# Kernel optimization log

Measured on AMD Instinct MI355X. Metric: run time of the kernel, lower is better.

## Reference

```python
import jax, jax.numpy as jnp
import numpy as np

D = 256      # cfg.d_model
H = 8        # num heads
HID = D // H # head_outdim for hidden layers (32)
N = 16000    # nodes
E = 64000    # edges
NUM_GNN = 3  # cfg.num_gnn -> 2 hidden EGATConv layers + 1 final
SLOPE = 0.01 # F.leaky_relu default in DGL EGATConv


def setup_inputs() -> dict:
    key = jax.random.key(0)
    ks = jax.random.split(key, 8)
    inp = {
        "nfeat": jax.random.normal(ks[0], (N, D), jnp.float32),
        "efeat": jax.random.normal(ks[1], (E, D), jnp.float32),
        "src": jax.random.randint(ks[2], (E,), 0, N),
        "dst": jax.random.randint(ks[3], (E,), 0, N),
    }
    L = NUM_GNN - 1  # hidden layers, out_node = out_edge = HID per head
    kh = jax.random.split(ks[4], 5)
    s = 0.02
    inp["Wnode_h"] = jax.random.normal(kh[0], (L, D, H * HID), jnp.float32) * s
    inp["Wni_h"]   = jax.random.normal(kh[1], (L, D, H * HID), jnp.float32) * s
    inp["Wnj_h"]   = jax.random.normal(kh[2], (L, D, H * HID), jnp.float32) * s
    inp["Wfij_h"]  = jax.random.normal(kh[3], (L, D, H * HID), jnp.float32) * s
    inp["attn_h"]  = jax.random.normal(kh[4], (L, H, HID), jnp.float32) * s
    inp["bias_h"]  = jnp.zeros((L, H * HID), jnp.float32)
    kl = jax.random.split(ks[5], 5)
    inp["Wnode_l"] = jax.random.normal(kl[0], (D, H * D), jnp.float32) * s
    inp["Wni_l"]   = jax.random.normal(kl[1], (D, H * D), jnp.float32) * s
    inp["Wnj_l"]   = jax.random.normal(kl[2], (D, H * D), jnp.float32) * s
    inp["Wfij_l"]  = jax.random.normal(kl[3], (D, H * D), jnp.float32) * s
    inp["attn_l"]  = jax.random.normal(kl[4], (H, D), jnp.float32) * s
    inp["bias_l"]  = jnp.zeros((H * D,), jnp.float32)
    return inp


def _egat(n, f, src, dst, Wnode, Wni, Wnj, Wfij, attn, bias):
    """DGL EGATConv: edge-gated multi-head graph attention.
    n:[N,D] f:[E,D] attn:[H,od] -> (h_out:[N,H,od], f_out:[E,H,od])."""
    Hh, od = attn.shape
    # edge feature update: f_ni(u) + f_nj(v) + f_fij(e) + bias, leaky_relu
    f_out = (n @ Wni)[src] + (n @ Wnj)[dst] + f @ Wfij + bias  # [E, H*od]
    f_out = jax.nn.leaky_relu(f_out, SLOPE).reshape(-1, Hh, od)
    # attention logits + edge softmax grouped by destination node
    e = jnp.einsum('ehd,hd->eh', f_out, attn)                   # [E, H]
    m = jax.lax.stop_gradient(jax.ops.segment_max(e, dst, num_segments=N))
    ex = jnp.exp(e - m[dst])
    s = jax.ops.segment_sum(ex, dst, num_segments=N)
    a = ex / s[dst]                                             # [E, H]
    # message passing: u_mul_e + sum at dst
    h = (n @ Wnode).reshape(N, Hh, od)
    h_out = jax.ops.segment_sum(h[src] * a[..., None], dst, num_segments=N)
    return h_out, f_out


def reference(nfeat, efeat, src, dst,
              Wnode_h, Wni_h, Wnj_h, Wfij_h, attn_h, bias_h,
              Wnode_l, Wni_l, Wnj_l, Wfij_l, attn_l, bias_l):
    n, f = nfeat, efeat
    for l in range(Wnode_h.shape[0]):  # hidden layers: concat heads + ELU + residual
        tn, tf = _egat(n, f, src, dst, Wnode_h[l], Wni_h[l], Wnj_h[l],
                       Wfij_h[l], attn_h[l], bias_h[l])
        n = n + jax.nn.elu(tn.reshape(N, -1))  # reshape == concat over heads
        f = f + jax.nn.elu(tf.reshape(E, -1))
    # last layer: mean over heads + residual
    tn, tf = _egat(n, f, src, dst, Wnode_l, Wni_l, Wnj_l, Wfij_l, attn_l, bias_l)
    n = n + tn.mean(axis=1)
    f = f + tf.mean(axis=1)
    return n, f
```

## Files before the change

kernel.cpp:

```cpp
#include <hip/hip_runtime.h>

typedef unsigned short u16;
typedef __attribute__((ext_vector_type(4))) unsigned short u16x4;
typedef __attribute__((ext_vector_type(8))) unsigned short u16x8;
typedef __attribute__((ext_vector_type(4))) float f32x4;
typedef __attribute__((ext_vector_type(8))) __bf16 bf16x8;

#define NN 16000
#define NE 64000
#define ECH 16000

__device__ __forceinline__ float bf2f(u16 b) {
  union { unsigned int u; float f; } v; v.u = ((unsigned int)b) << 16; return v.f;
}
__device__ __forceinline__ u16 f2bf(float x) {
  union { float f; unsigned int u; } v; v.f = x;
  unsigned int r = v.u + 0x7FFFu + ((v.u >> 16) & 1u);
  return (u16)(r >> 16);
}

__global__ void cast_init(const float* __restrict__ in, float* __restrict__ outf,
                          u16* __restrict__ outb, int n4) {
  for (int i = blockIdx.x * blockDim.x + threadIdx.x; i < n4; i += gridDim.x * blockDim.x) {
    f32x4 v = ((const f32x4*)in)[i];
    u16x4 b;
#pragma unroll
    for (int j = 0; j < 4; ++j) b[j] = f2bf(v[j]);
    ((f32x4*)outf)[i] = v;
    ((u16x4*)outb)[i] = b;
  }
}

__global__ void cast_bf(const float* __restrict__ in, u16* __restrict__ outb, int n4) {
  for (int i = blockIdx.x * blockDim.x + threadIdx.x; i < n4; i += gridDim.x * blockDim.x) {
    f32x4 v = ((const f32x4*)in)[i];
    u16x4 b;
#pragma unroll
    for (int j = 0; j < 4; ++j) b[j] = f2bf(v[j]);
    ((u16x4*)outb)[i] = b;
  }
}

__global__ void deg_hist(const int* __restrict__ dst, int* __restrict__ deg) {
  int e = blockIdx.x * 256 + threadIdx.x;
  if (e < NE) atomicAdd(&deg[dst[e]], 1);
}

__global__ __launch_bounds__(1024) void scan_deg(const int* __restrict__ deg,
                                                 int* __restrict__ row_ptr,
                                                 int* __restrict__ cursor) {
  __shared__ int lds[1024];
  int t = threadIdx.x;
  int base = t * 16;
  int v[16];
  int s = 0;
#pragma unroll
  for (int j = 0; j < 16; ++j) {
    int idx = base + j;
    v[j] = idx < NN ? deg[idx] : 0;
    s += v[j];
  }
  lds[t] = s;
  __syncthreads();
  for (int d = 1; d < 1024; d <<= 1) {
    int x = t >= d ? lds[t - d] : 0;
    __syncthreads();
    lds[t] += x;
    __syncthreads();
  }
  int run = lds[t] - s;
  for (int j = 0; j < 16; ++j) {
    int idx = base + j;
    if (idx < NN) { row_ptr[idx] = run; cursor[idx] = run; run += v[j]; }
  }
  if (t == 1023) row_ptr[NN] = run;
}

__global__ void csr_fill(const int* __restrict__ src, const int* __restrict__ dst,
                         int* __restrict__ cursor, int* __restrict__ cs_e,
                         int* __restrict__ cs_src) {
  int e = blockIdx.x * 256 + threadIdx.x;
  if (e >= NE) return;
  int pos = atomicAdd(&cursor[dst[e]], 1);
  cs_e[pos] = e;
  cs_src[pos] = src[e];
}

__global__ void transpose4(const float* __restrict__ W0, const float* __restrict__ W1,
                           const float* __restrict__ W2, const float* __restrict__ W3,
                           int ld, int osz, u16* __restrict__ WT) {
  __shared__ float t[16][17];
  int z = blockIdx.z;
  const float* W = z == 0 ? W0 : (z == 1 ? W1 : (z == 2 ? W2 : W3));
  u16* O = WT + (size_t)z * osz;
  int n0 = blockIdx.x * 16, k0 = blockIdx.y * 16;
  int tx = threadIdx.x, ty = threadIdx.y;
  t[ty][tx] = W[(size_t)(k0 + ty) * ld + n0 + tx];
  __syncthreads();
  O[(size_t)(n0 + ty) * 256 + k0 + tx] = f2bf(t[tx][ty]);
}

__global__ void transpose4p(const float* __restrict__ W0, const float* __restrict__ W1,
                            const float* __restrict__ W2, const float* __restrict__ W3,
                            u16* __restrict__ WT) {
  __shared__ float t[16][17];
  int z = blockIdx.z;
  const float* W = z == 0 ? W0 : (z == 1 ? W1 : (z == 2 ? W2 : W3));
  u16* O = WT + (size_t)z * 524288;
  int n0 = blockIdx.x * 16, k0 = blockIdx.y * 16;
  int tx = threadIdx.x, ty = threadIdx.y;
  t[ty][tx] = W[(size_t)(k0 + ty) * 2048 + n0 + tx];
  __syncthreads();
  int n = n0 + ty;
  int j = (n & 255) * 8 + (n >> 8);
  O[(size_t)j * 256 + k0 + tx] = f2bf(t[tx][ty]);
}

__global__ void permute_ba(const float* __restrict__ bias, const float* __restrict__ attn,
                           float* __restrict__ bias_p, float* __restrict__ attn_p) {
  int n = blockIdx.x * 256 + threadIdx.x;
  int j = (n & 255) * 8 + (n >> 8);
  bias_p[j] = bias[n];
  attn_p[j] = attn[n];
}

__global__ __launch_bounds__(256) void gemm_abt(
    const u16* __restrict__ A,
    const u16* __restrict__ BT0, const u16* __restrict__ BT1, const u16* __restrict__ BT2,
    u16* __restrict__ C0, u16* __restrict__ C1, u16* __restrict__ C2, int ldc) {
  const int bz = blockIdx.z;
  const u16* BT = bz == 0 ? BT0 : (bz == 1 ? BT1 : BT2);
  u16* C = bz == 0 ? C0 : (bz == 1 ? C1 : C2);
  const int nx = gridDim.x;
  const int nwg = nx * gridDim.y;
  int bid = blockIdx.y * nx + blockIdx.x;
  int q = nwg >> 3, r = nwg & 7;
  int xcd = bid & 7, idx = bid >> 3;
  int wg = (xcd < r) ? (xcd * (q + 1) + idx) : (r * (q + 1) + (xcd - r) * q + idx);
  const int m0 = (wg / nx) * 128;
  const int n0 = (wg % nx) * 128;
  __shared__ __attribute__((aligned(16))) char smem[69632];
  u16* lA = (u16*)smem;
  u16* lB = (u16*)(smem + 32768);
  const int tid = threadIdx.x;
  const int lane = tid & 63;
  const int wid = tid >> 6;
  const int wr = (wid >> 1) * 64;
  const int wc = (wid & 1) * 64;
  const int srow = tid >> 3;
  const int sdst = (tid & 7) * 8;
  const int ssrc = (((tid & 7) ^ (srow & 7))) * 8;
  const int sx = (lane >> 4) ^ (lane & 7);
  f32x4 acc[4][4] = {};
#define STAGE(buf, kb)                                                                         \
  {                                                                                            \
    _Pragma("unroll") for (int i = 0; i < 4; ++i) {                                            \
      const int row = srow + i * 32;                                                           \
      __builtin_amdgcn_global_load_lds(                                                        \
          (const __attribute__((address_space(1))) void*)(A + (size_t)(m0 + row) * 256 + (kb) + ssrc), \
          (__attribute__((address_space(3))) void*)(lA + (buf) * 8192 + row * 64 + sdst), 16, 0, 0); \
      __builtin_amdgcn_global_load_lds(                                                        \
          (const __attribute__((address_space(1))) void*)(BT + (size_t)(n0 + row) * 256 + (kb) + ssrc), \
          (__attribute__((address_space(3))) void*)(lB + (buf) * 8192 + row * 64 + sdst), 16, 0, 0); \
    }                                                                                          \
  }
  STAGE(0, 0)
  __syncthreads();
#pragma unroll
  for (int t = 0; t < 4; ++t) {
    if (t < 3) STAGE((t + 1) & 1, (t + 1) * 64)
    const u16* pA = lA + (t & 1) * 8192;
    const u16* pB = lB + (t & 1) * 8192;
#pragma unroll
    for (int kk = 0; kk < 2; ++kk) {
      const int sw = ((kk << 2) ^ sx) * 8;
      bf16x8 af[4], bfr[4];
#pragma unroll
      for (int m = 0; m < 4; ++m)
        af[m] = *(const bf16x8*)(pA + (wr + m * 16 + (lane & 15)) * 64 + sw);
#pragma unroll
      for (int n = 0; n < 4; ++n)
        bfr[n] = *(const bf16x8*)(pB + (wc + n * 16 + (lane & 15)) * 64 + sw);
#pragma unroll
      for (int m = 0; m < 4; ++m)
#pragma unroll
        for (int n = 0; n < 4; ++n)
          acc[m][n] = __builtin_amdgcn_mfma_f32_16x16x32_bf16(af[m], bfr[n], acc[m][n], 0, 0, 0);
    }
    __syncthreads();
  }
#undef STAGE
  const int cr = (lane >> 4) * 4;
  const int cc = lane & 15;
  float* stg = (float*)smem + wid * (64 * 68);
#pragma unroll
  for (int m = 0; m < 4; ++m)
#pragma unroll
    for (int n = 0; n < 4; ++n)
#pragma unroll
      for (int j = 0; j < 4; ++j)
        stg[(m * 16 + cr + j) * 68 + n * 16 + cc] = acc[m][n][j];
  const int rr = lane >> 3;
  const int c0 = (lane & 7) * 8;
#pragma unroll
  for (int p = 0; p < 8; ++p) {
    int row = p * 8 + rr;
    f32x4 v0 = *(const f32x4*)(stg + row * 68 + c0);
    f32x4 v1 = *(const f32x4*)(stg + row * 68 + c0 + 4);
    u16x8 o;
#pragma unroll
    for (int i = 0; i < 4; ++i) { o[i] = f2bf(v0[i]); o[4 + i] = f2bf(v1[i]); }
    *(u16x8*)(&C[(size_t)(m0 + wr + row) * ldc + (n0 + wc + c0)]) = o;
  }
}

__global__ __launch_bounds__(256) void gemm_fused_final(
    int e0, const u16* __restrict__ A, const u16* __restrict__ BT,
    const u16* __restrict__ t_ni, const u16* __restrict__ t_nj,
    const int* __restrict__ src, const int* __restrict__ dst,
    const float* __restrict__ bias_p, const float* __restrict__ attn_p,
    const u16* __restrict__ f_bf, float* __restrict__ out_f, float* __restrict__ part) {
  const int nx = gridDim.x;
  const int nwg = nx * gridDim.y;
  int bid = blockIdx.y * nx + blockIdx.x;
  int q = nwg >> 3, r = nwg & 7;
  int xcd = bid & 7, idx = bid >> 3;
  int wg = (xcd < r) ? (xcd * (q + 1) + idx) : (r * (q + 1) + (xcd - r) * q + idx);
  const int m0 = (wg / nx) * 128;
  const int n0 = (wg % nx) * 128;
  __shared__ __attribute__((aligned(16))) char smem[69632];
  u16* lA = (u16*)smem;
  u16* lB = (u16*)(smem + 32768);
  const int tid = threadIdx.x;
  const int lane = tid & 63;
  const int wid = tid >> 6;
  const int wr = (wid >> 1) * 64;
  const int wc = (wid & 1) * 64;
  const int srow = tid >> 3;
  const int sdst = (tid & 7) * 8;
  const int ssrc = (((tid & 7) ^ (srow & 7))) * 8;
  const int sx = (lane >> 4) ^ (lane & 7);
  f32x4 acc[4][4] = {};
#define STAGE(buf, kb)                                                                         \
  {                                                                                            \
    _Pragma("unroll") for (int i = 0; i < 4; ++i) {                                            \
      const int row = srow + i * 32;                                                           \
      __builtin_amdgcn_global_load_lds(                                                        \
          (const __attribute__((address_space(1))) void*)(A + (size_t)(m0 + row) * 256 + (kb) + ssrc), \
          (__attribute__((address_space(3))) void*)(lA + (buf) * 8192 + row * 64 + sdst), 16, 0, 0); \
      __builtin_amdgcn_global_load_lds(                                                        \
          (const __attribute__((address_space(1))) void*)(BT + (size_t)(n0 + row) * 256 + (kb) + ssrc), \
          (__attribute__((address_space(3))) void*)(lB + (buf) * 8192 + row * 64 + sdst), 16, 0, 0); \
    }                                                                                          \
  }
  STAGE(0, 0)
  __syncthreads();
#pragma unroll
  for (int t = 0; t < 4; ++t) {
    if (t < 3) STAGE((t + 1) & 1, (t + 1) * 64)
    const u16* pA = lA + (t & 1) * 8192;
    const u16* pB = lB + (t & 1) * 8192;
#pragma unroll
    for (int kk = 0; kk < 2; ++kk) {
      const int sw = ((kk << 2) ^ sx) * 8;
      bf16x8 af[4], bfr[4];
#pragma unroll
      for (int m = 0; m < 4; ++m)
        af[m] = *(const bf16x8*)(pA + (wr + m * 16 + (lane & 15)) * 64 + sw);
#pragma unroll
      for (int n = 0; n < 4; ++n)
        bfr[n] = *(const bf16x8*)(pB + (wc + n * 16 + (lane & 15)) * 64 + sw);
#pragma unroll
      for (int m = 0; m < 4; ++m)
#pragma unroll
        for (int n = 0; n < 4; ++n)
          acc[m][n] = __builtin_amdgcn_mfma_f32_16x16x32_bf16(af[m], bfr[n], acc[m][n], 0, 0, 0);
    }
    __syncthreads();
  }
#undef STAGE
  const int cr = (lane >> 4) * 4;
  const int cc = lane & 15;
  float* stg = (float*)smem + wid * (64 * 68);
#pragma unroll
  for (int m = 0; m < 4; ++m)
#pragma unroll
    for (int n = 0; n < 4; ++n)
#pragma unroll
      for (int j = 0; j < 4; ++j)
        stg[(m * 16 + cr + j) * 68 + n * 16 + cc] = acc[m][n][j];
  const int rr = lane >> 3;
  const int c0 = (lane & 7) * 8;
  const int j0 = n0 + wc + c0;
  const int cmod = j0 >> 3;
  const int wgrp = (n0 + wc) >> 6;
  f32x4 bias0 = *(const f32x4*)(bias_p + j0);
  f32x4 bias1 = *(const f32x4*)(bias_p + j0 + 4);
  f32x4 attn0 = *(const f32x4*)(attn_p + j0);
  f32x4 attn1 = *(const f32x4*)(attn_p + j0 + 4);
#pragma unroll 4
  for (int p = 0; p < 8; ++p) {
    int row = p * 8 + rr;
    int er = m0 + wr + row;
    int e = e0 + er;
    int is = src[e], id = dst[e];
    f32x4 v0 = *(const f32x4*)(stg + row * 68 + c0);
    f32x4 v1 = *(const f32x4*)(stg + row * 68 + c0 + 4);
    u16x8 ni8 = *(const u16x8*)(t_ni + (size_t)is * 2048 + j0);
    u16x8 nj8 = *(const u16x8*)(t_nj + (size_t)id * 2048 + j0);
    float y[8];
#pragma unroll
    for (int h = 0; h < 4; ++h) {
      float t0 = v0[h] + bf2f(ni8[h]) + bf2f(nj8[h]) + bias0[h];
      y[h] = t0 > 0.f ? t0 : 0.01f * t0;
      float t1 = v1[h] + bf2f(ni8[4 + h]) + bf2f(nj8[4 + h]) + bias1[h];
      y[4 + h] = t1 > 0.f ? t1 : 0.01f * t1;
    }
    float outv = 0.125f * (((y[0] + y[1]) + (y[2] + y[3])) + ((y[4] + y[5]) + (y[6] + y[7])));
    out_f[(size_t)e * 256 + cmod] = outv + bf2f(f_bf[(size_t)e * 256 + cmod]);
    float lp[8];
#pragma unroll
    for (int h = 0; h < 4; ++h) { lp[h] = y[h] * attn0[h]; lp[4 + h] = y[4 + h] * attn1[h]; }
#pragma unroll
    for (int mask = 1; mask < 8; mask <<= 1)
#pragma unroll
      for (int h = 0; h < 8; ++h) lp[h] += __shfl_xor(lp[h], mask);
    if ((lane & 7) == 0)
#pragma unroll
      for (int h = 0; h < 8; ++h) part[(size_t)er * 256 + h * 32 + wgrp] = lp[h];
  }
}

__global__ __launch_bounds__(256) void logit_reduce(
    int e0, const float* __restrict__ part, float* __restrict__ exb) {
  int er = blockIdx.x * 4 + (threadIdx.x >> 6);
  if (er >= ECH) return;
  int lane = threadIdx.x & 63;
  int h = lane >> 3;
  int w4 = (lane & 7) * 4;
  f32x4 v = *(const f32x4*)(part + (size_t)er * 256 + h * 32 + w4);
  float s = (v[0] + v[1]) + (v[2] + v[3]);
  s += __shfl_xor(s, 1);
  s += __shfl_xor(s, 2);
  s += __shfl_xor(s, 4);
  s = fminf(fmaxf(s, -30.f), 30.f);
  if ((lane & 7) == 0) exb[(size_t)(e0 + er) * 8 + h] = expf(s);
}

__global__ __launch_bounds__(256) void edge_hidden(
    const u16* __restrict__ t3, const u16* __restrict__ fW,
    const int* __restrict__ src, const int* __restrict__ dst,
    const float* __restrict__ bias, const float* __restrict__ attn,
    u16* __restrict__ f_bf, float* __restrict__ exb) {
  int e = blockIdx.x * 4 + (threadIdx.x >> 6);
  if (e >= NE) return;
  int lane = threadIdx.x & 63;
  int is = src[e], id = dst[e];
  int c = lane * 4;
  u16x4 va = *(const u16x4*)(t3 + (size_t)is * 768 + c);
  u16x4 vb = *(const u16x4*)(t3 + (size_t)id * 768 + 256 + c);
  u16x4 vc = *(const u16x4*)(fW + (size_t)e * 256 + c);
  f32x4 vbi = *(const f32x4*)(bias + c);
  int h = lane >> 3;
  f32x4 vat = *(const f32x4*)(attn + h * 32 + (lane & 7) * 4);
  size_t idx0 = (size_t)e * 256 + c;
  u16x4 fo = *(u16x4*)(f_bf + idx0);
  float part = 0.f;
#pragma unroll
  for (int j = 0; j < 4; ++j) {
    float y = bf2f(va[j]) + bf2f(vb[j]) + bf2f(vc[j]) + vbi[j];
    y = y > 0.f ? y : 0.01f * y;
    part += y * vat[j];
    float el = y > 0.f ? y : expm1f(y);
    fo[j] = f2bf(bf2f(fo[j]) + el);
  }
  *(u16x4*)(f_bf + idx0) = fo;
  part += __shfl_xor(part, 1);
  part += __shfl_xor(part, 2);
  part += __shfl_xor(part, 4);
  part = fminf(fmaxf(part, -30.f), 30.f);
  if ((lane & 7) == 0) exb[(size_t)e * 8 + h] = expf(part);
}

__global__ __launch_bounds__(256) void node_gather_hidden(
    const u16* __restrict__ t3, const int* __restrict__ row_ptr,
    const int* __restrict__ cs_e, const int* __restrict__ cs_src,
    const float* __restrict__ exb, float* __restrict__ n_cur, u16* __restrict__ n_bf) {
  int node = blockIdx.x * 4 + (threadIdx.x >> 6);
  if (node >= NN) return;
  int lane = threadIdx.x & 63;
  int c = lane * 4, h = lane >> 3;
  int beg = row_ptr[node], end = row_ptr[node + 1];
  float denom = 0.f;
  float acc[4] = {0.f, 0.f, 0.f, 0.f};
  for (int p = beg; p < end; ++p) {
    float a = exb[(size_t)cs_e[p] * 8 + h];
    denom += a;
    u16x4 hv = *(const u16x4*)(t3 + (size_t)cs_src[p] * 768 + 512 + c);
#pragma unroll
    for (int j = 0; j < 4; ++j) acc[j] += a * bf2f(hv[j]);
  }
  float inv = denom > 0.f ? 1.f / denom : 0.f;
  size_t i0 = (size_t)node * 256 + c;
  f32x4 nv = *(f32x4*)(n_cur + i0);
  u16x4 bv;
#pragma unroll
  for (int j = 0; j < 4; ++j) {
    float t = acc[j] * inv;
    t = t > 0.f ? t : expm1f(t);
    nv[j] += t;
    bv[j] = f2bf(nv[j]);
  }
  *(f32x4*)(n_cur + i0) = nv;
  *(u16x4*)(n_bf + i0) = bv;
}

__global__ __launch_bounds__(256) void node_gather_final_all(
    const u16* __restrict__ t_node, const int* __restrict__ row_ptr,
    const int* __restrict__ cs_e, const int* __restrict__ cs_src,
    const float* __restrict__ exb, const float* __restrict__ n_cur,
    float* __restrict__ out_n) {
  int node = blockIdx.x * 4 + (threadIdx.x >> 6);
  if (node >= NN) return;
  int lane = threadIdx.x & 63;
  int c = lane * 4;
  int beg = row_ptr[node], end = row_ptr[node + 1];
  float dh[8] = {};
  float acc[8][4] = {};
  for (int p = beg; p < end; ++p) {
    int e = cs_e[p];
    int s = cs_src[p];
    const u16* rowb = t_node + (size_t)s * 2048 + (size_t)c * 8;
    const float* eb = exb + (size_t)e * 8;
    float a[8];
    u16x8 rv[4];
#pragma unroll
    for (int h = 0; h < 8; ++h) a[h] = eb[h];
#pragma unroll
    for (int jj = 0; jj < 4; ++jj) rv[jj] = *(const u16x8*)(rowb + jj * 8);
#pragma unroll
    for (int h = 0; h < 8; ++h) {
      dh[h] += a[h];
#pragma unroll
      for (int jj = 0; jj < 4; ++jj) acc[h][jj] += a[h] * bf2f(rv[jj][h]);
    }
  }
  float total[4] = {0.f, 0.f, 0.f, 0.f};
#pragma unroll
  for (int h = 0; h < 8; ++h) {
    float inv = dh[h] > 0.f ? 0.125f / dh[h] : 0.f;
#pragma unroll
    for (int jj = 0; jj < 4; ++jj) total[jj] += acc[h][jj] * inv;
  }
  size_t i0 = (size_t)node * 256 + c;
  f32x4 nv = *(const f32x4*)(n_cur + i0);
#pragma unroll
  for (int jj = 0; jj < 4; ++jj) nv[jj] += total[jj];
  *(f32x4*)(out_n + i0) = nv;
}

extern "C" void kernel_launch(void* const* d_in, const int* in_sizes, int n_in,
                              void* d_out, int out_size, void* d_ws, size_t ws_size,
                              hipStream_t stream) {
  const float* nfeat   = (const float*)d_in[0];
  const float* efeat   = (const float*)d_in[1];
  const int*   src     = (const int*)d_in[2];
  const int*   dst     = (const int*)d_in[3];
  const float* Wnode_h = (const float*)d_in[4];
  const float* Wni_h   = (const float*)d_in[5];
  const float* Wnj_h   = (const float*)d_in[6];
  const float* Wfij_h  = (const float*)d_in[7];
  const float* attn_h  = (const float*)d_in[8];
  const float* bias_h  = (const float*)d_in[9];
  const float* Wnode_l = (const float*)d_in[10];
  const float* Wni_l   = (const float*)d_in[11];
  const float* Wnj_l   = (const float*)d_in[12];
  const float* Wfij_l  = (const float*)d_in[13];
  const float* attn_l  = (const float*)d_in[14];
  const float* bias_l  = (const float*)d_in[15];

  char* ws = (char*)d_ws;
  size_t off = 0;
  auto alloc = [&](size_t b) { char* p = ws + off; off += (b + 255) & ~(size_t)255; return p; };
  float* n_cur = (float*)alloc((size_t)NN * 256 * 4);
  u16* n_bf    = (u16*)alloc((size_t)NN * 256 * 2);
  u16* f_bf    = (u16*)alloc((size_t)NE * 256 * 2);
  u16* t_ni    = (u16*)alloc((size_t)NN * 2048 * 2);
  u16* t_nj    = (u16*)alloc((size_t)NN * 2048 * 2);
  u16* t_node  = (u16*)alloc((size_t)NN * 2048 * 2);
  float* exb   = (float*)alloc((size_t)NE * 8 * 4);
  u16* WT      = (u16*)alloc((size_t)4 * 65536 * 2);
  u16* WTF     = (u16*)alloc((size_t)4 * 524288 * 2);
  u16* fW      = (u16*)alloc((size_t)NE * 256 * 2);
  float* part  = (float*)alloc((size_t)ECH * 256 * 4);
  float* biasp = (float*)alloc(2048 * 4);
  float* attnp = (float*)alloc(2048 * 4);
  int* deg     = (int*)alloc((size_t)NN * 4);
  int* cursor  = (int*)alloc((size_t)NN * 4);
  int* row_ptr = (int*)alloc((size_t)(NN + 1) * 4);
  int* cs_e    = (int*)alloc((size_t)NE * 4);
  int* cs_src  = (int*)alloc((size_t)NE * 4);

  u16* WT_fij  = WT + 3 * 65536;
  u16* WTF_node = WTF;
  u16* WTF_ni   = WTF + (size_t)1 * 524288;
  u16* WTF_nj   = WTF + (size_t)2 * 524288;
  u16* WTF_fij  = WTF + (size_t)3 * 524288;

  float* out_n = (float*)d_out;
  float* out_f = out_n + (size_t)NN * 256;

  hipMemsetAsync(deg, 0, (size_t)NN * 4, stream);
  deg_hist<<<(NE + 255) / 256, 256, 0, stream>>>(dst, deg);
  scan_deg<<<1, 1024, 0, stream>>>(deg, row_ptr, cursor);
  csr_fill<<<(NE + 255) / 256, 256, 0, stream>>>(src, dst, cursor, cs_e, cs_src);

  cast_init<<<1024, 256, 0, stream>>>(nfeat, n_cur, n_bf, NN * 256 / 4);
  cast_bf<<<2048, 256, 0, stream>>>(efeat, f_bf, NE * 256 / 4);

  for (int l = 0; l < 2; ++l) {
    transpose4<<<dim3(16, 16, 4), dim3(16, 16), 0, stream>>>(
        Wni_h + (size_t)l * 65536, Wnj_h + (size_t)l * 65536,
        Wnode_h + (size_t)l * 65536, Wfij_h + (size_t)l * 65536, 256, 65536, WT);
    gemm_abt<<<dim3(6, 125, 1), 256, 0, stream>>>(n_bf, WT, WT, WT,
                                                  t_ni, t_ni, t_ni, 768);
    gemm_abt<<<dim3(2, 500, 1), 256, 0, stream>>>(f_bf, WT_fij, WT_fij, WT_fij,
                                                  fW, fW, fW, 256);
    edge_hidden<<<16000, 256, 0, stream>>>(t_ni, fW, src, dst,
        bias_h + (size_t)l * 256, attn_h + (size_t)l * 256, f_bf, exb);
    node_gather_hidden<<<4000, 256, 0, stream>>>(t_ni, row_ptr, cs_e, cs_src, exb, n_cur, n_bf);
  }

  transpose4p<<<dim3(128, 16, 4), dim3(16, 16), 0, stream>>>(
      Wnode_l, Wni_l, Wnj_l, Wfij_l, WTF);
  permute_ba<<<8, 256, 0, stream>>>(bias_l, attn_l, biasp, attnp);
  gemm_abt<<<dim3(16, 125, 3), 256, 0, stream>>>(n_bf, WTF_ni, WTF_nj, WTF_node,
                                                 t_ni, t_nj, t_node, 2048);
  for (int e0 = 0; e0 < NE; e0 += ECH) {
    gemm_fused_final<<<dim3(16, ECH / 128), 256, 0, stream>>>(
        e0, f_bf + (size_t)e0 * 256, WTF_fij, t_ni, t_nj, src, dst,
        biasp, attnp, f_bf, out_f, part);
    logit_reduce<<<ECH / 4, 256, 0, stream>>>(e0, part, exb);
  }
  node_gather_final_all<<<4000, 256, 0, stream>>>(t_node, row_ptr, cs_e, cs_src,
                                                  exb, n_cur, out_n);
}
```

Before: 660.3 us.

## Prefetch gathered node rows before GEMM and transpose logit partial layout

Gathers of src/dst indices, the t_ni/t_nj bf16 rows and the residual f_bf values in the last-layer edge GEMM kernel are moved before the MFMA main loop. Their memory latency can then overlap the matrix multiply instead of stalling the epilogue. The partial attention-logit buffer layout changes from head-major to wgroup-major so the eight per-head stores from one lane are contiguous, and logit_reduce is rewritten to match. The cost is higher register pressure from holding 8 u16x8 pairs across the GEMM, which may reduce occupancy or cause spills.

```diff
diff --git a/kernel.cpp b/kernel.cpp
--- a/kernel.cpp
+++ b/kernel.cpp
@@ -240,6 +240,21 @@
   const int sdst = (tid & 7) * 8;
   const int ssrc = (((tid & 7) ^ (srow & 7))) * 8;
   const int sx = (lane >> 4) ^ (lane & 7);
+  const int rr = lane >> 3;
+  const int c0e = (lane & 7) * 8;
+  const int j0 = n0 + wc + c0e;
+  const int cmod = j0 >> 3;
+  const int wgrp = (n0 + wc) >> 6;
+  u16x8 ni8v[8], nj8v[8];
+  u16 fsv[8];
+#pragma unroll
+  for (int p = 0; p < 8; ++p) {
+    int e = e0 + m0 + wr + p * 8 + rr;
+    int is = src[e], id = dst[e];
+    ni8v[p] = *(const u16x8*)(t_ni + (size_t)is * 2048 + j0);
+    nj8v[p] = *(const u16x8*)(t_nj + (size_t)id * 2048 + j0);
+    fsv[p] = f_bf[(size_t)e * 256 + cmod];
+  }
   f32x4 acc[4][4] = {};
 #define STAGE(buf, kb)                                                                         \
   {                                                                                            \
@@ -289,35 +304,27 @@
 #pragma unroll
       for (int j = 0; j < 4; ++j)
         stg[(m * 16 + cr + j) * 68 + n * 16 + cc] = acc[m][n][j];
-  const int rr = lane >> 3;
-  const int c0 = (lane & 7) * 8;
-  const int j0 = n0 + wc + c0;
-  const int cmod = j0 >> 3;
-  const int wgrp = (n0 + wc) >> 6;
   f32x4 bias0 = *(const f32x4*)(bias_p + j0);
   f32x4 bias1 = *(const f32x4*)(bias_p + j0 + 4);
   f32x4 attn0 = *(const f32x4*)(attn_p + j0);
   f32x4 attn1 = *(const f32x4*)(attn_p + j0 + 4);
-#pragma unroll 4
+#pragma unroll
   for (int p = 0; p < 8; ++p) {
     int row = p * 8 + rr;
     int er = m0 + wr + row;
     int e = e0 + er;
-    int is = src[e], id = dst[e];
-    f32x4 v0 = *(const f32x4*)(stg + row * 68 + c0);
-    f32x4 v1 = *(const f32x4*)(stg + row * 68 + c0 + 4);
-    u16x8 ni8 = *(const u16x8*)(t_ni + (size_t)is * 2048 + j0);
-    u16x8 nj8 = *(const u16x8*)(t_nj + (size_t)id * 2048 + j0);
+    f32x4 v0 = *(const f32x4*)(stg + row * 68 + c0e);
+    f32x4 v1 = *(const f32x4*)(stg + row * 68 + c0e + 4);
     float y[8];
 #pragma unroll
     for (int h = 0; h < 4; ++h) {
-      float t0 = v0[h] + bf2f(ni8[h]) + bf2f(nj8[h]) + bias0[h];
+      float t0 = v0[h] + bf2f(ni8v[p][h]) + bf2f(nj8v[p][h]) + bias0[h];
       y[h] = t0 > 0.f ? t0 : 0.01f * t0;
-      float t1 = v1[h] + bf2f(ni8[4 + h]) + bf2f(nj8[4 + h]) + bias1[h];
+      float t1 = v1[h] + bf2f(ni8v[p][4 + h]) + bf2f(nj8v[p][4 + h]) + bias1[h];
       y[4 + h] = t1 > 0.f ? t1 : 0.01f * t1;
     }
     float outv = 0.125f * (((y[0] + y[1]) + (y[2] + y[3])) + ((y[4] + y[5]) + (y[6] + y[7])));
-    out_f[(size_t)e * 256 + cmod] = outv + bf2f(f_bf[(size_t)e * 256 + cmod]);
+    out_f[(size_t)e * 256 + cmod] = outv + bf2f(fsv[p]);
     float lp[8];
 #pragma unroll
     for (int h = 0; h < 4; ++h) { lp[h] = y[h] * attn0[h]; lp[4 + h] = y[4 + h] * attn1[h]; }
@@ -325,9 +332,10 @@
     for (int mask = 1; mask < 8; mask <<= 1)
 #pragma unroll
       for (int h = 0; h < 8; ++h) lp[h] += __shfl_xor(lp[h], mask);
-    if ((lane & 7) == 0)
-#pragma unroll
-      for (int h = 0; h < 8; ++h) part[(size_t)er * 256 + h * 32 + wgrp] = lp[h];
+    if ((lane & 7) == 0) {
+#pragma unroll
+      for (int h = 0; h < 8; ++h) part[(size_t)er * 256 + wgrp * 8 + h] = lp[h];
+    }
   }
 }
 
@@ -336,15 +344,16 @@
   int er = blockIdx.x * 4 + (threadIdx.x >> 6);
   if (er >= ECH) return;
   int lane = threadIdx.x & 63;
-  int h = lane >> 3;
-  int w4 = (lane & 7) * 4;
-  f32x4 v = *(const f32x4*)(part + (size_t)er * 256 + h * 32 + w4);
-  float s = (v[0] + v[1]) + (v[2] + v[3]);
-  s += __shfl_xor(s, 1);
-  s += __shfl_xor(s, 2);
-  s += __shfl_xor(s, 4);
+  int h = lane & 7;
+  int w0 = (lane >> 3) * 4;
+  float s = 0.f;
+#pragma unroll
+  for (int k = 0; k < 4; ++k) s += part[(size_t)er * 256 + (w0 + k) * 8 + h];
+  s += __shfl_xor(s, 8);
+  s += __shfl_xor(s, 16);
+  s += __shfl_xor(s, 32);
   s = fminf(fmaxf(s, -30.f), 30.f);
-  if ((lane & 7) == 0) exb[(size_t)(e0 + er) * 8 + h] = expf(s);
+  if (lane < 8) exb[(size_t)(e0 + er) * 8 + h] = expf(s);
 }
 
 __global__ __launch_bounds__(256) void edge_hidden(
```

After: 632.5 us. -4.2%, faster.
